# Kernel optimization log

Hardware: AMD Instinct MI355X
Metric: run time of the kernel (lower is better)

## Reference

```python
import jax, jax.numpy as jnp
import numpy as np

B = 16384        # batch of states
D_IN = 512       # num_inputs (= num_gating_input)
H0 = 1024        # hidden_layer[0]
H1 = 1024        # hidden_layer[1]
D_OUT = 64       # num_outputs
E = 8            # num_experts (hard-coded in module)
G_H = 128        # gate MLP hidden width


def setup_inputs() -> dict:
    key = jax.random.key(0)
    ks = jax.random.split(key, 14)
    s = 0.05
    return {
        "inputs": jax.random.normal(ks[0], (B, D_IN), dtype=jnp.float32),
        # gate MLP: Linear(D_IN,128) -> relu -> Linear(128,128) -> relu -> Linear(128,E)
        "gw1": jax.random.normal(ks[1], (D_IN, G_H), dtype=jnp.float32) * s,
        "gb1": jnp.zeros((G_H,), dtype=jnp.float32),
        "gw2": jax.random.normal(ks[2], (G_H, G_H), dtype=jnp.float32) * s,
        "gb2": jnp.zeros((G_H,), dtype=jnp.float32),
        "gw3": jax.random.normal(ks[3], (G_H, E), dtype=jnp.float32) * s,
        "gb3": jnp.zeros((E,), dtype=jnp.float32),
        # expert (policy) layers: (weight [E,in,out], bias [E,1,out])
        "w0": jax.random.normal(ks[4], (E, D_IN, H0), dtype=jnp.float32) * s,
        "b0": jax.random.normal(ks[5], (E, 1, H0), dtype=jnp.float32) * s,
        "w1": jax.random.normal(ks[6], (E, H0, H1), dtype=jnp.float32) * s,
        "b1": jax.random.normal(ks[7], (E, 1, H1), dtype=jnp.float32) * s,
        "w2": jax.random.normal(ks[8], (E, H1, D_OUT), dtype=jnp.float32) * s,
        "b2": jax.random.normal(ks[9], (E, 1, D_OUT), dtype=jnp.float32) * s,
    }


def reference(inputs, gw1, gb1, gw2, gb2, gw3, gb3, w0, b0, w1, b1, w2, b2):
    # Gate: softmax over experts, torch code reshapes to [E, B, 1] via .t().unsqueeze(-1);
    # here keep g as [B, E] and contract the expert axis directly.
    h = jax.nn.relu(inputs @ gw1 + gb1)
    h = jax.nn.relu(h @ gw2 + gb2)
    g = jax.nn.softmax(h @ gw3 + gb3, axis=1)  # [B, E]

    def expert_layer(x, w, b, act):
        # out.matmul(weight) : [B,d] x [E,d,h] -> [E,B,h]; +bias; *gate; sum over E
        y = jnp.einsum('bd,edh->ebh', x, w) + b      # [E, B, h]
        return act(jnp.einsum('be,ebh->bh', g, y))   # [B, h]

    x = expert_layer(inputs, w0, b0, jax.nn.relu)
    x = expert_layer(x, w1, b1, jax.nn.relu)
    x = expert_layer(x, w2, b2, jnp.tanh)
    return x
```

## Files before the change

### kernel.cpp

```cpp
#include <hip/hip_runtime.h>
#include <hip/hip_bf16.h>
#include <cstdint>

#define DI __device__ __forceinline__

typedef unsigned short ushort_t;
using u16x8  = __attribute__((ext_vector_type(8))) unsigned short;
using bf16x8 = __attribute__((ext_vector_type(8))) __bf16;
using f32x4  = __attribute__((ext_vector_type(4))) float;

typedef const __attribute__((address_space(1))) void GVOID;
typedef __attribute__((address_space(3))) void LVOID;

enum { BB = 16384, DIN = 512, H0 = 1024, H1 = 1024, DOUT = 64, NE = 8, GH = 128 };

DI void async_ld16(const void* g, void* l) {
    __builtin_amdgcn_global_load_lds((GVOID*)g, (LVOID*)l, 16, 0, 0);
}

DI unsigned short f2bf(float f) {
    union { float f; unsigned u; } v; v.f = f;
    unsigned r = v.u + 0x7FFF + ((v.u >> 16) & 1);
    return (unsigned short)(r >> 16);
}
DI float bf2f(unsigned short u) { return __uint_as_float(((unsigned)u) << 16); }
DI f32x4 zero4() { f32x4 v = {0.f, 0.f, 0.f, 0.f}; return v; }

#define BARRIER() do { __builtin_amdgcn_s_barrier(); asm volatile("" ::: "memory"); } while (0)
#define LGKM0()   asm volatile("s_waitcnt lgkmcnt(0)" ::: "memory")

__global__ void f32_to_bf16_vec(const float* __restrict__ in, ushort_t* __restrict__ out) {
    const int i = (blockIdx.x * 256 + threadIdx.x) * 8;
    const float4 a = *(const float4*)&in[i];
    const float4 b = *(const float4*)&in[i + 4];
    u16x8 o;
    o[0] = f2bf(a.x); o[1] = f2bf(a.y); o[2] = f2bf(a.z); o[3] = f2bf(a.w);
    o[4] = f2bf(b.x); o[5] = f2bf(b.y); o[6] = f2bf(b.z); o[7] = f2bf(b.w);
    *(u16x8*)&out[i] = o;
}

__global__ void transpose_convert(const float* __restrict__ W, ushort_t* __restrict__ Wt,
                                  int K, int N, int Kext) {
    __shared__ float t[64][69];
    const int tid = threadIdx.x;
    const int k0 = blockIdx.x * 64, n0 = blockIdx.y * 64;
    for (int rr = tid >> 4; rr < 64; rr += 16) {
        const int c = (tid & 15) * 4;
        const float4 v = *(const float4*)&W[(size_t)(k0 + rr) * N + n0 + c];
        t[rr][c] = v.x; t[rr][c + 1] = v.y; t[rr][c + 2] = v.z; t[rr][c + 3] = v.w;
    }
    __syncthreads();
    for (int nn = tid >> 3; nn < 64; nn += 32) {
        const int k8 = (tid & 7) * 8;
        u16x8 o;
#pragma unroll
        for (int j = 0; j < 8; ++j) o[j] = f2bf(t[k8 + j][nn]);
        *(u16x8*)&Wt[(size_t)(n0 + nn) * Kext + k0 + k8] = o;
    }
}

__global__ void bias_fill(const float* __restrict__ bias, ushort_t* __restrict__ Wt,
                          int N, int K, int Kext) {
    const int n = blockIdx.x, c = threadIdx.x;
    Wt[(size_t)n * Kext + K + c] = (c < 8) ? f2bf(bias[(size_t)c * N + n]) : (ushort_t)0;
}

__global__ void gate3_softmax(const ushort_t* __restrict__ h2, const float* __restrict__ gw3,
                              const float* __restrict__ gb3, float* __restrict__ g,
                              ushort_t* __restrict__ Gx) {
    __shared__ float w[GH * NE];
    const int tid = threadIdx.x;
    for (int i = tid; i < GH * NE; i += 256) w[i] = gw3[i];
    __syncthreads();
    const int b = blockIdx.x * 256 + tid;
    float lg[NE];
#pragma unroll
    for (int e = 0; e < NE; ++e) lg[e] = gb3[e];
    const ushort_t* row = h2 + (size_t)b * GH;
    for (int h8 = 0; h8 < GH; h8 += 8) {
        const u16x8 v = *(const u16x8*)&row[h8];
#pragma unroll
        for (int j = 0; j < 8; ++j) {
            const float xv = bf2f(v[j]);
#pragma unroll
            for (int e = 0; e < NE; ++e) lg[e] += xv * w[(h8 + j) * NE + e];
        }
    }
    float mx = lg[0];
#pragma unroll
    for (int e = 1; e < NE; ++e) mx = fmaxf(mx, lg[e]);
    float s = 0.f;
#pragma unroll
    for (int e = 0; e < NE; ++e) { lg[e] = __expf(lg[e] - mx); s += lg[e]; }
    const float inv = 1.f / s;
#pragma unroll
    for (int e = 0; e < NE; ++e) g[(size_t)b * NE + e] = lg[e] * inv;
    ushort_t* gxr = Gx + (size_t)b * 128;
    u16x8 o;
#pragma unroll
    for (int e = 0; e < NE; ++e) o[e] = f2bf(lg[e] * inv);
    *(u16x8*)gxr = o;
    u16x8 z = {0, 0, 0, 0, 0, 0, 0, 0};
#pragma unroll
    for (int i = 1; i < 16; ++i) *(u16x8*)(gxr + i * 8) = z;
}

template <int TPE64, int STRIDEX>
__global__ __launch_bounds__(512, 2) void gemm256p(
    const ushort_t* __restrict__ X,
    const ushort_t* __restrict__ Gx,
    const ushort_t* __restrict__ Wt,
    const float* __restrict__ gvec,
    ushort_t* __restrict__ out,
    int N, int Kext) {
    constexpr int TE64 = NE * TPE64;
    const int NT = Kext >> 6;
    const int tid = threadIdx.x;
    const int wid = tid >> 6, l = tid & 63;
    const int wm = wid >> 2, wn = wid & 3;
    const int lr = l & 15, lk = l >> 4;

    const int b = blockIdx.x;
    const int xcd = b & 7, j2 = b >> 3;
    const int by = j2 & 3, bx = xcd + 8 * (j2 >> 2);
    const int bm0 = bx * 256, bn0 = by * 256;

    __shared__ __align__(1024) char lA[2][2][16384];
    __shared__ __align__(1024) char lB[2][2][16384];
    __shared__ float rtab[256 * 8];

    for (int r = tid; r < 256; r += 512) {
        const float* gr = gvec + (size_t)(bm0 + r) * 8;
        float ge[8];
#pragma unroll
        for (int e = 0; e < 8; ++e) ge[e] = gr[e];
#pragma unroll
        for (int e = 0; e < 7; ++e) rtab[r * 8 + e] = ge[e] / ge[e + 1];
        rtab[r * 8 + 7] = ge[7];
    }

    const int srow = (wid << 3) + (l >> 3);
    const int scol = (((l & 7) ^ (srow & 7)) << 3);
    auto stA = [&](int t, int h) {
        char* dst = (char*)lA[t & 1][h] + (wid << 10);
        if (t < TE64) {
            const ushort_t* s = X + (size_t)(bm0 + h * 128 + srow) * STRIDEX
                                  + (t & (TPE64 - 1)) * 64 + scol;
            async_ld16(s, dst);
            async_ld16(s + (size_t)64 * STRIDEX, dst + 8192);
        } else {
            const ushort_t* s = Gx + (size_t)(bm0 + h * 128 + srow) * 128
                                   + (t - TE64) * 64 + scol;
            async_ld16(s, dst);
            async_ld16(s + 64 * 128, dst + 8192);
        }
    };
    auto stB = [&](int t, int h) {
        char* dst = (char*)lB[t & 1][h] + (wid << 10);
        const ushort_t* s = Wt + (size_t)(bn0 + h * 128 + srow) * (size_t)Kext
                              + t * 64 + scol;
        async_ld16(s, dst);
        async_ld16(s + (size_t)64 * Kext, dst + 8192);
    };

    const int chunk0 = ((lk ^ (lr & 7)) << 4);
    const int aoff = lr * 128;
    const int boff = ((wn & 1) << 13) + lr * 128;

    f32x4 acc[8][4];
#pragma unroll
    for (int m = 0; m < 8; ++m)
#pragma unroll
        for (int n = 0; n < 4; ++n) acc[m][n] = zero4();

    stB(0, 0); stB(0, 1); stA(0, 0); stA(0, 1);
    stB(1, 0); stB(1, 1); stA(1, 0); stA(1, 1);
    LGKM0();
    asm volatile("s_waitcnt vmcnt(8)" ::: "memory");
    BARRIER();

    for (int t = 0; t < NT; ++t) {
        const char* Ah = (const char*)lA[t & 1][wm] + aoff;
        const char* Bh = (const char*)lB[t & 1][wn >> 1] + boff;
        bf16x8 a0[4], a1[4], b0[2], b1[2], b2f[2], b3f[2];

#pragma unroll
        for (int m = 0; m < 4; ++m) {
            a0[m] = *(const bf16x8*)(Ah + m * 2048 + chunk0);
            a1[m] = *(const bf16x8*)(Ah + m * 2048 + (chunk0 ^ 64));
        }
#pragma unroll
        for (int n = 0; n < 2; ++n) {
            b0[n] = *(const bf16x8*)(Bh + n * 2048 + chunk0);
            b1[n] = *(const bf16x8*)(Bh + n * 2048 + (chunk0 ^ 64));
        }
        asm volatile("s_waitcnt lgkmcnt(8)" ::: "memory");
        BARRIER();
        LGKM0();
        __builtin_amdgcn_s_setprio(1);
#pragma unroll
        for (int m = 0; m < 4; ++m)
#pragma unroll
            for (int n = 0; n < 2; ++n) {
                acc[m][n] = __builtin_amdgcn_mfma_f32_16x16x32_bf16(a0[m], b0[n], acc[m][n], 0, 0, 0);
                acc[m][n] = __builtin_amdgcn_mfma_f32_16x16x32_bf16(a1[m], b1[n], acc[m][n], 0, 0, 0);
            }
        __builtin_amdgcn_s_setprio(0);
        BARRIER();

#pragma unroll
        for (int n = 0; n < 2; ++n) {
            b2f[n] = *(const bf16x8*)(Bh + (n + 2) * 2048 + chunk0);
            b3f[n] = *(const bf16x8*)(Bh + (n + 2) * 2048 + (chunk0 ^ 64));
        }
        BARRIER();
        LGKM0();
        __builtin_amdgcn_s_setprio(1);
#pragma unroll
        for (int m = 0; m < 4; ++m)
#pragma unroll
            for (int n = 0; n < 2; ++n) {
                acc[m][n + 2] = __builtin_amdgcn_mfma_f32_16x16x32_bf16(a0[m], b2f[n], acc[m][n + 2], 0, 0, 0);
                acc[m][n + 2] = __builtin_amdgcn_mfma_f32_16x16x32_bf16(a1[m], b3f[n], acc[m][n + 2], 0, 0, 0);
            }
        __builtin_amdgcn_s_setprio(0);
        BARRIER();

#pragma unroll
        for (int m = 0; m < 4; ++m) {
            a0[m] = *(const bf16x8*)(Ah + (m + 4) * 2048 + chunk0);
            a1[m] = *(const bf16x8*)(Ah + (m + 4) * 2048 + (chunk0 ^ 64));
        }
        if (t + 2 < NT) { stB(t + 2, 0); stB(t + 2, 1); }
        BARRIER();
        LGKM0();
        __builtin_amdgcn_s_setprio(1);
#pragma unroll
        for (int m = 0; m < 4; ++m)
#pragma unroll
            for (int n = 0; n < 2; ++n) {
                acc[m + 4][n] = __builtin_amdgcn_mfma_f32_16x16x32_bf16(a0[m], b0[n], acc[m + 4][n], 0, 0, 0);
                acc[m + 4][n] = __builtin_amdgcn_mfma_f32_16x16x32_bf16(a1[m], b1[n], acc[m + 4][n], 0, 0, 0);
            }
        __builtin_amdgcn_s_setprio(0);
        BARRIER();

        if (t + 2 < NT) { stA(t + 2, 0); stA(t + 2, 1); }
        BARRIER();
        __builtin_amdgcn_s_setprio(1);
#pragma unroll
        for (int m = 0; m < 4; ++m)
#pragma unroll
            for (int n = 0; n < 2; ++n) {
                acc[m + 4][n + 2] = __builtin_amdgcn_mfma_f32_16x16x32_bf16(a0[m], b2f[n], acc[m + 4][n + 2], 0, 0, 0);
                acc[m + 4][n + 2] = __builtin_amdgcn_mfma_f32_16x16x32_bf16(a1[m], b3f[n], acc[m + 4][n + 2], 0, 0, 0);
            }
        __builtin_amdgcn_s_setprio(0);

        if (t < TE64 && ((t + 1) & (TPE64 - 1)) == 0) {
            const int e = t / TPE64;
#pragma unroll
            for (int m = 0; m < 8; ++m)
#pragma unroll
                for (int q = 0; q < 4; ++q) {
                    const float r = rtab[(wm * 128 + m * 16 + lk * 4 + q) * 8 + e];
#pragma unroll
                    for (int n = 0; n < 4; ++n) acc[m][n][q] *= r;
                }
        }
        if (t + 2 < NT) {
            asm volatile("s_waitcnt vmcnt(8)" ::: "memory");
            BARRIER();
        } else if (t + 1 < NT) {
            asm volatile("s_waitcnt vmcnt(0)" ::: "memory");
            BARRIER();
        }
    }

#pragma unroll
    for (int m = 0; m < 8; ++m) {
        const int row = bm0 + wm * 128 + m * 16 + lk * 4;
#pragma unroll
        for (int n = 0; n < 4; ++n) {
            const int col = bn0 + wn * 64 + n * 16 + lr;
#pragma unroll
            for (int q = 0; q < 4; ++q) {
                const float v = fmaxf(acc[m][n][q], 0.f);
                out[(size_t)(row + q) * N + col] = f2bf(v);
            }
        }
    }
}

template <int BN, int TPE, int ACT, bool GATED, bool OUTF32>
__global__ __launch_bounds__(256, 2) void moe_gemm(
    const ushort_t* __restrict__ X, const ushort_t* __restrict__ Wt,
    const float* __restrict__ gvec, const float* __restrict__ bias,
    void* __restrict__ outv, int M, int N, int K, int Klen) {
    constexpr int BM = 128, BK = 64;
    constexpr int NF = BN / 32;
    const int tid = threadIdx.x;
    const int wid = tid >> 6, lane = tid & 63;
    const int lr = lane & 15, lk = lane >> 4;
    const int bm0 = blockIdx.x * BM;
    const int bn0 = blockIdx.y * BN;
    const int wm0 = (wid >> 1) * 64;
    const int wn0 = (wid & 1) * (BN / 2);
    const int koff = blockIdx.z * Klen;
    const int te0 = (TPE > 0) ? koff / (TPE * BK) : 0;

    __shared__ short lds_a[BM * BK];
    __shared__ short lds_b[BN * BK];
    __shared__ float lds_g[BM * 8];
    __shared__ float lds_bias[8 * BN];

    if constexpr (GATED) {
        ((f32x4*)lds_g)[tid] = ((const f32x4*)(gvec + (size_t)bm0 * 8))[tid];
        if constexpr (ACT != 2) {
            for (int i = tid; i < 8 * BN; i += 256) {
                const int e = i / BN, n = i - e * BN;
                lds_bias[i] = bias[(size_t)e * N + bn0 + n];
            }
        }
    }

    f32x4 acc_t[4][NF], acc_p[4][NF];
#pragma unroll
    for (int m = 0; m < 4; ++m)
#pragma unroll
        for (int n = 0; n < NF; ++n) { acc_t[m][n] = zero4(); acc_p[m][n] = zero4(); }

    f32x4(&amain)[4][NF] = GATED ? acc_p : acc_t;

    const int xstride = (TPE > 0) ? TPE * BK : K;
    const int NT = Klen / BK;
    for (int kt = 0; kt < NT; ++kt) {
        int kcolA;
        if constexpr (TPE > 0) kcolA = (kt % TPE) * BK; else kcolA = kt * BK;
        {
            const ushort_t* abase = X + (size_t)bm0 * xstride + kcolA;
#pragma unroll
            for (int c = wid; c < (BM * BK * 2) / 1024; c += 4) {
                const int off = c * 1024 + lane * 16;
                const int r = off >> 7, cbyte = off & 127;
                async_ld16((const char*)abase + (size_t)r * (xstride * 2) + cbyte,
                           (char*)lds_a + c * 1024);
            }
            const ushort_t* bbase = Wt + (size_t)bn0 * K + koff + kt * BK;
#pragma unroll
            for (int c = wid; c < (BN * BK * 2) / 1024; c += 4) {
                const int off = c * 1024 + lane * 16;
                const int r = off >> 7, cbyte = off & 127;
                async_ld16((const char*)bbase + (size_t)r * ((size_t)K * 2) + cbyte,
                           (char*)lds_b + c * 1024);
            }
        }
        __syncthreads();

        bf16x8 af[2][4], bfr[2][NF];
#pragma unroll
        for (int k2 = 0; k2 < 2; ++k2) {
#pragma unroll
            for (int m = 0; m < 4; ++m)
                af[k2][m] = *(const bf16x8*)&lds_a[(wm0 + m * 16 + lr) * BK + k2 * 32 + lk * 8];
#pragma unroll
            for (int n = 0; n < NF; ++n)
                bfr[k2][n] = *(const bf16x8*)&lds_b[(wn0 + n * 16 + lr) * BK + k2 * 32 + lk * 8];
        }
#pragma unroll
        for (int m = 0; m < 4; ++m)
#pragma unroll
            for (int n = 0; n < NF; ++n) {
                amain[m][n] = __builtin_amdgcn_mfma_f32_16x16x32_bf16(af[0][m], bfr[0][n], amain[m][n], 0, 0, 0);
                amain[m][n] = __builtin_amdgcn_mfma_f32_16x16x32_bf16(af[1][m], bfr[1][n], amain[m][n], 0, 0, 0);
            }

        if constexpr (TPE > 0 && GATED) {
            if ((kt + 1) % TPE == 0) {
                const int e = te0 + kt / TPE;
#pragma unroll
                for (int m = 0; m < 4; ++m)
#pragma unroll
                    for (int q = 0; q < 4; ++q) {
                        const float gw = lds_g[(wm0 + m * 16 + lk * 4 + q) * 8 + e];
#pragma unroll
                        for (int n = 0; n < NF; ++n) {
                            acc_t[m][n][q] += gw * acc_p[m][n][q];
                            acc_p[m][n][q] = 0.f;
                        }
                    }
            }
        }
        __syncthreads();
    }

#pragma unroll
    for (int m = 0; m < 4; ++m)
#pragma unroll
        for (int n = 0; n < NF; ++n)
#pragma unroll
            for (int q = 0; q < 4; ++q) {
                const int row = wm0 + m * 16 + lk * 4 + q;
                const int col = wn0 + n * 16 + lr;
                float v = acc_t[m][n][q];
                if constexpr (ACT != 2) {
                    if constexpr (GATED) {
                        float bs = 0.f;
#pragma unroll
                        for (int e = 0; e < 8; ++e) bs += lds_g[row * 8 + e] * lds_bias[e * BN + col];
                        v += bs;
                    } else {
                        v += bias[bn0 + col];
                    }
                }
                if constexpr (ACT == 0) v = fmaxf(v, 0.f);
                else if constexpr (ACT == 1) v = tanhf(v);
                const size_t oidx = (size_t)blockIdx.z * M * N + (size_t)(bm0 + row) * N + (bn0 + col);
                if constexpr (OUTF32) ((float*)outv)[oidx] = v;
                else ((ushort_t*)outv)[oidx] = f2bf(v);
            }
}

__global__ void splitk_reduce8(const float* __restrict__ part, const float* __restrict__ g,
                               const float* __restrict__ b2, float* __restrict__ out) {
    __shared__ float bs[8 * 64];
    const int tid = threadIdx.x;
    for (int i = tid; i < 512; i += 256) bs[i] = b2[i];
    __syncthreads();
    const int idx = blockIdx.x * 256 + tid;
    const int bb = idx >> 6, n = idx & 63;
    const float* gr = g + (size_t)bb * 8;
    float v = 0.f;
#pragma unroll
    for (int e = 0; e < 8; ++e)
        v += gr[e] * (part[(size_t)e * BB * 64 + idx] + bs[e * 64 + n]);
    out[idx] = tanhf(v);
}

extern "C" void kernel_launch(void* const* d_in, const int* in_sizes, int n_in,
                              void* d_out, int out_size, void* d_ws, size_t ws_size,
                              hipStream_t stream) {
    const float* inputs = (const float*)d_in[0];
    const float* gw1 = (const float*)d_in[1];
    const float* gb1 = (const float*)d_in[2];
    const float* gw2 = (const float*)d_in[3];
    const float* gb2 = (const float*)d_in[4];
    const float* gw3 = (const float*)d_in[5];
    const float* gb3 = (const float*)d_in[6];
    const float* w0 = (const float*)d_in[7];
    const float* b0 = (const float*)d_in[8];
    const float* w1 = (const float*)d_in[9];
    const float* b1 = (const float*)d_in[10];
    const float* w2 = (const float*)d_in[11];
    const float* b2 = (const float*)d_in[12];
    (void)in_sizes; (void)n_in; (void)out_size; (void)ws_size;

    constexpr int KE0 = NE * DIN + 128;
    constexpr int KE1 = NE * H0 + 128;

    char* ws = (char*)d_ws;
    ushort_t* x0b = (ushort_t*)(ws + 0);
    ushort_t* W0t = (ushort_t*)(ws + 16777216);
    ushort_t* G1t = (ushort_t*)(ws + 25427968);
    ushort_t* G2t = (ushort_t*)(ws + 25559040);
    ushort_t* h1b = (ushort_t*)(ws + 25591808);
    ushort_t* h2b = (ushort_t*)(ws + 29786112);
    ushort_t* x2b = (ushort_t*)(ws + 0);
    ushort_t* W1t = (ushort_t*)(ws + 33980416);
    ushort_t* W2t = (ushort_t*)(ws + 51019776);
    float*    gv  = (float*)(ws + 52068352);
    ushort_t* Gx  = (ushort_t*)(ws + 52592640);
    ushort_t* x1b = (ushort_t*)(ws + 56786944);
    float*    p2  = (float*)(ws + 56786944);

    f32_to_bf16_vec<<<dim3((BB * DIN) / (256 * 8)), 256, 0, stream>>>(inputs, x0b);
    transpose_convert<<<dim3((NE * DIN) / 64, H0 / 64), 256, 0, stream>>>(w0, W0t, NE * DIN, H0, KE0);
    transpose_convert<<<dim3((NE * H0) / 64, H1 / 64), 256, 0, stream>>>(w1, W1t, NE * H0, H1, KE1);
    transpose_convert<<<dim3((NE * H1) / 64, DOUT / 64), 256, 0, stream>>>(w2, W2t, NE * H1, DOUT, NE * H1);
    transpose_convert<<<dim3(DIN / 64, GH / 64), 256, 0, stream>>>(gw1, G1t, DIN, GH, DIN);
    transpose_convert<<<dim3(GH / 64, GH / 64), 256, 0, stream>>>(gw2, G2t, GH, GH, GH);
    bias_fill<<<dim3(H0), 128, 0, stream>>>(b0, W0t, H0, NE * DIN, KE0);
    bias_fill<<<dim3(H1), 128, 0, stream>>>(b1, W1t, H1, NE * H0, KE1);

    moe_gemm<128, 0, 0, false, false><<<dim3(BB / 128, GH / 128), 256, 0, stream>>>(
        x0b, G1t, nullptr, gb1, h1b, BB, GH, DIN, DIN);
    moe_gemm<128, 0, 0, false, false><<<dim3(BB / 128, GH / 128), 256, 0, stream>>>(
        h1b, G2t, nullptr, gb2, h2b, BB, GH, GH, GH);
    gate3_softmax<<<dim3(BB / 256), 256, 0, stream>>>(h2b, gw3, gb3, gv, Gx);

    gemm256p<DIN / 64, DIN><<<dim3((BB / 256) * (H0 / 256)), 512, 0, stream>>>(
        x0b, Gx, W0t, gv, x1b, H0, KE0);
    gemm256p<H0 / 64, H0><<<dim3((BB / 256) * (H1 / 256)), 512, 0, stream>>>(
        x1b, Gx, W1t, gv, x2b, H1, KE1);

    moe_gemm<64, 16, 2, false, true><<<dim3(BB / 128, DOUT / 64, 8), 256, 0, stream>>>(
        x2b, W2t, nullptr, nullptr, p2, BB, DOUT, NE * H1, H1);
    splitk_reduce8<<<dim3((BB * DOUT) / 256), 256, 0, stream>>>(p2, gv, b2, (float*)d_out);
}
```

Measured before the change: 460.5 us.

## Merge GEMM main-loop phases and shorten A-tile prefetch distance to one

The GEMM main loop now reads all four B fragments at once and runs two MFMA phases per K-step instead of four, which removes several block-wide barriers and LDS wait points. The prefetch of A tiles moves from two K-steps ahead at the end of the iteration to one K-step ahead at the start, so the prologue no longer preloads the second A tile. The vmcnt waits are adjusted to match the new number of outstanding loads. The aim is less synchronisation overhead per K-step, at the cost of a shorter window in which to hide A global-load latency.

Measured after the change: 441.7 us. -4.1%, faster.

```diff
diff --git a/kernel.cpp b/kernel.cpp
--- a/kernel.cpp
+++ b/kernel.cpp
@@ -174,15 +174,15 @@
         for (int n = 0; n < 4; ++n) acc[m][n] = zero4();
 
     stB(0, 0); stB(0, 1); stA(0, 0); stA(0, 1);
-    stB(1, 0); stB(1, 1); stA(1, 0); stA(1, 1);
+    stB(1, 0); stB(1, 1);
     LGKM0();
-    asm volatile("s_waitcnt vmcnt(8)" ::: "memory");
+    asm volatile("s_waitcnt vmcnt(4)" ::: "memory");
     BARRIER();
 
     for (int t = 0; t < NT; ++t) {
         const char* Ah = (const char*)lA[t & 1][wm] + aoff;
         const char* Bh = (const char*)lB[t & 1][wn >> 1] + boff;
-        bf16x8 a0[4], a1[4], b0[2], b1[2], b2f[2], b3f[2];
+        bf16x8 a0[4], a1[4], b0[4], b1[4];
 
 #pragma unroll
         for (int m = 0; m < 4; ++m) {
@@ -190,10 +190,11 @@
             a1[m] = *(const bf16x8*)(Ah + m * 2048 + (chunk0 ^ 64));
         }
 #pragma unroll
-        for (int n = 0; n < 2; ++n) {
+        for (int n = 0; n < 4; ++n) {
             b0[n] = *(const bf16x8*)(Bh + n * 2048 + chunk0);
             b1[n] = *(const bf16x8*)(Bh + n * 2048 + (chunk0 ^ 64));
         }
+        if (t + 1 < NT) { stA(t + 1, 0); stA(t + 1, 1); }
         asm volatile("s_waitcnt lgkmcnt(8)" ::: "memory");
         BARRIER();
         LGKM0();
@@ -201,27 +202,9 @@
 #pragma unroll
         for (int m = 0; m < 4; ++m)
 #pragma unroll
-            for (int n = 0; n < 2; ++n) {
+            for (int n = 0; n < 4; ++n) {
                 acc[m][n] = __builtin_amdgcn_mfma_f32_16x16x32_bf16(a0[m], b0[n], acc[m][n], 0, 0, 0);
                 acc[m][n] = __builtin_amdgcn_mfma_f32_16x16x32_bf16(a1[m], b1[n], acc[m][n], 0, 0, 0);
-            }
-        __builtin_amdgcn_s_setprio(0);
-        BARRIER();
-
-#pragma unroll
-        for (int n = 0; n < 2; ++n) {
-            b2f[n] = *(const bf16x8*)(Bh + (n + 2) * 2048 + chunk0);
-            b3f[n] = *(const bf16x8*)(Bh + (n + 2) * 2048 + (chunk0 ^ 64));
-        }
-        BARRIER();
-        LGKM0();
-        __builtin_amdgcn_s_setprio(1);
-#pragma unroll
-        for (int m = 0; m < 4; ++m)
-#pragma unroll
-            for (int n = 0; n < 2; ++n) {
-                acc[m][n + 2] = __builtin_amdgcn_mfma_f32_16x16x32_bf16(a0[m], b2f[n], acc[m][n + 2], 0, 0, 0);
-                acc[m][n + 2] = __builtin_amdgcn_mfma_f32_16x16x32_bf16(a1[m], b3f[n], acc[m][n + 2], 0, 0, 0);
             }
         __builtin_amdgcn_s_setprio(0);
         BARRIER();
@@ -238,24 +221,11 @@
 #pragma unroll
         for (int m = 0; m < 4; ++m)
 #pragma unroll
-            for (int n = 0; n < 2; ++n) {
+            for (int n = 0; n < 4; ++n) {
                 acc[m + 4][n] = __builtin_amdgcn_mfma_f32_16x16x32_bf16(a0[m], b0[n], acc[m + 4][n], 0, 0, 0);
                 acc[m + 4][n] = __builtin_amdgcn_mfma_f32_16x16x32_bf16(a1[m], b1[n], acc[m + 4][n], 0, 0, 0);
             }
         __builtin_amdgcn_s_setprio(0);
-        BARRIER();
-
-        if (t + 2 < NT) { stA(t + 2, 0); stA(t + 2, 1); }
-        BARRIER();
-        __builtin_amdgcn_s_setprio(1);
-#pragma unroll
-        for (int m = 0; m < 4; ++m)
-#pragma unroll
-            for (int n = 0; n < 2; ++n) {
-                acc[m + 4][n + 2] = __builtin_amdgcn_mfma_f32_16x16x32_bf16(a0[m], b2f[n], acc[m + 4][n + 2], 0, 0, 0);
-                acc[m + 4][n + 2] = __builtin_amdgcn_mfma_f32_16x16x32_bf16(a1[m], b3f[n], acc[m + 4][n + 2], 0, 0, 0);
-            }
-        __builtin_amdgcn_s_setprio(0);
 
         if (t < TE64 && ((t + 1) & (TPE64 - 1)) == 0) {
             const int e = t / TPE64;
@@ -269,7 +239,7 @@
                 }
         }
         if (t + 2 < NT) {
-            asm volatile("s_waitcnt vmcnt(8)" ::: "memory");
+            asm volatile("s_waitcnt vmcnt(4)" ::: "memory");
             BARRIER();
         } else if (t + 1 < NT) {
             asm volatile("s_waitcnt vmcnt(0)" ::: "memory");
```
